# Kernel tuning notes

Hardware: AMD Instinct MI355X
Metric: run time of the kernel (lower is better)

The kernel has to match this reference:

```python
import jax, jax.numpy as jnp
import numpy as np
from jax.scipy.special import logsumexp

N_STATES = 512
N_OBS = 1024
BATCH = 64
T_MAX = 512


def setup_inputs() -> dict:
    key = jax.random.key(0)
    k1, k2, k3, k4, k5 = jax.random.split(key, 5)
    pi = jnp.zeros((N_STATES,), dtype=jnp.float32)
    A = jax.random.normal(k1, (N_STATES, N_STATES), dtype=jnp.float32)  # unnormalized transition
    E = jax.random.normal(k2, (N_STATES, N_OBS), dtype=jnp.float32)     # unnormalized emission
    x = jax.random.randint(k3, (BATCH, T_MAX), 0, N_OBS)
    T = jax.random.randint(k4, (BATCH,), 1, T_MAX + 1)
    return {"pi": pi, "A": A, "E": E, "x": x, "T": T}


def reference(pi, A, E, x, T):
    # log p(x) via forward algorithm in log domain.
    log_pi = jax.nn.log_softmax(pi)                # (N,)
    log_A = jax.nn.log_softmax(A, axis=0)          # (N,N), matches torch dim=0
    log_E = jax.nn.log_softmax(E, axis=1)          # (N,M)

    # emission log-probs per timestep: (B, T_max, N)
    log_em = jnp.moveaxis(log_E[:, x], 0, -1)

    alpha0 = log_em[:, 0, :] + log_pi              # (B,N)

    def step(carry, em_t):
        # carry: (B,N) over k; log_A: (N_i, N_k)
        # next[b,i] = em_t[b,i] + logsumexp_k(log_A[i,k] + carry[b,k])
        nxt = em_t + logsumexp(log_A[None, :, :] + carry[:, None, :], axis=2)
        return nxt, nxt

    em_rest = jnp.swapaxes(log_em[:, 1:, :], 0, 1)  # (T_max-1, B, N)
    _, alphas = jax.lax.scan(step, alpha0, em_rest)
    log_alpha = jnp.concatenate([alpha0[:, None, :], jnp.swapaxes(alphas, 0, 1)], axis=1)  # (B,T_max,N)

    log_sums = logsumexp(log_alpha, axis=2)         # (B, T_max)
    log_probs = jnp.take_along_axis(log_sums, (T - 1)[:, None], axis=1)  # (B,1)
    return log_probs
```

## Files before the change

kernel.cpp:

```cpp
#include <hip/hip_runtime.h>
#include <math.h>

#define NS   512
#define NO   1024
#define NB   64
#define TMAX 512

#define QREG 45
#define QLDS 19

typedef _Float16 h2v __attribute__((ext_vector_type(2)));

__device__ inline float wave_red_sum(float x) {
#pragma unroll
  for (int o = 32; o; o >>= 1) x += __shfl_xor(x, o, 64);
  return x;
}
__device__ inline float wave_red_max(float x) {
#pragma unroll
  for (int o = 32; o; o >>= 1) x = fmaxf(x, __shfl_xor(x, o, 64));
  return x;
}

__device__ inline float dot2u(unsigned int a, unsigned int b, float c) {
#if __has_builtin(__builtin_amdgcn_fdot2)
  return __builtin_amdgcn_fdot2(__builtin_bit_cast(h2v, a),
                                __builtin_bit_cast(h2v, b), c, false);
#else
  h2v av = __builtin_bit_cast(h2v, a), bv = __builtin_bit_cast(h2v, b);
  return c + (float)av.x * (float)bv.x + (float)av.y * (float)bv.y;
#endif
}

__global__ void k_pi(const float* __restrict__ pi, float* __restrict__ pi_sm) {
  __shared__ float red[8];
  int tid = threadIdx.x;
  float v = pi[tid];
  float m = wave_red_max(v);
  if ((tid & 63) == 0) red[tid >> 6] = m;
  __syncthreads();
  m = fmaxf(fmaxf(fmaxf(red[0], red[1]), fmaxf(red[2], red[3])),
            fmaxf(fmaxf(red[4], red[5]), fmaxf(red[6], red[7])));
  float e = __expf(v - m);
  float s = wave_red_sum(e);
  __syncthreads();
  if ((tid & 63) == 0) red[tid >> 6] = s;
  __syncthreads();
  s = red[0] + red[1] + red[2] + red[3] + red[4] + red[5] + red[6] + red[7];
  pi_sm[tid] = e / s;
}

__global__ void k_colLse(const float* __restrict__ A, float* __restrict__ lseA) {
  __shared__ float redm[4];
  __shared__ float reds[4];
  int k = blockIdx.x, tid = threadIdx.x;
  float a0 = A[tid * NS + k], a1 = A[(tid + 256) * NS + k];
  float m = wave_red_max(fmaxf(a0, a1));
  if ((tid & 63) == 0) redm[tid >> 6] = m;
  __syncthreads();
  m = fmaxf(fmaxf(redm[0], redm[1]), fmaxf(redm[2], redm[3]));
  float s = __expf(a0 - m) + __expf(a1 - m);
  s = wave_red_sum(s);
  if ((tid & 63) == 0) reds[tid >> 6] = s;
  __syncthreads();
  s = reds[0] + reds[1] + reds[2] + reds[3];
  if (tid == 0) lseA[k] = m + __logf(s);
}

__global__ void k_rowLseE(const float* __restrict__ E, float* __restrict__ lseE) {
  __shared__ float red[4];
  int i = blockIdx.x, tid = threadIdx.x;
  const float* row = E + i * NO;
  float a0 = row[tid], a1 = row[tid + 256], a2 = row[tid + 512], a3 = row[tid + 768];
  float m = fmaxf(fmaxf(a0, a1), fmaxf(a2, a3));
  m = wave_red_max(m);
  if ((tid & 63) == 0) red[tid >> 6] = m;
  __syncthreads();
  m = fmaxf(fmaxf(red[0], red[1]), fmaxf(red[2], red[3]));
  float s = __expf(a0 - m) + __expf(a1 - m) + __expf(a2 - m) + __expf(a3 - m);
  s = wave_red_sum(s);
  __syncthreads();
  if ((tid & 63) == 0) red[tid >> 6] = s;
  __syncthreads();
  s = red[0] + red[1] + red[2] + red[3];
  if (tid == 0) lseE[i] = m + __logf(s);
}

__global__ void k_pack(const float* __restrict__ A, const float* __restrict__ lseA,
                       unsigned int* __restrict__ W) {
  int u = blockIdx.x * 512 + threadIdx.x;
  int q = u >> 11;
  int r = u & 2047;
  int i = r >> 2;
  int h = r & 3;
  int k0 = q * 8 + h * 2;
  float e0 = __expf(A[i * NS + k0]     - lseA[k0]);
  float e1 = __expf(A[i * NS + k0 + 1] - lseA[k0 + 1]);
  h2v p;
  p.x = (_Float16)e0;
  p.y = (_Float16)e1;
  W[u] = __builtin_bit_cast(unsigned int, p);
}

__global__ __launch_bounds__(512, 1) void k_fwd(
    const float* __restrict__ E, const int* __restrict__ x,
    const int* __restrict__ Tlen, const float* __restrict__ pi_sm,
    const float* __restrict__ lseE, const uint4* __restrict__ Aall,
    float* __restrict__ out) {
  __shared__ uint4 Alds[QLDS * 512];
  __shared__ uint4 vbuf[2][NS / 8];
  __shared__ int xrow[TMAX];
  __shared__ float red[8];
  int b = blockIdx.x, tid = threadIdx.x;

  uint4 areg[QREG];
#pragma unroll
  for (int q = 0; q < QREG; q++) areg[q] = Aall[q * 512 + tid];
#pragma unroll
  for (int q = 0; q < QLDS; q++) Alds[q * 512 + tid] = Aall[(QREG + q) * 512 + tid];

  for (int t = tid; t < TMAX; t += 512) xrow[t] = x[b * TMAX + t];

  float pi_i  = pi_sm[tid];
  float lse_i = lseE[tid];
  const float* Erow = E + tid * NO;
  int Tb = Tlen[b];
  float c = 0.f;
  int cur = 0;
  __syncthreads();

  for (int t = 0; t < Tb; t++) {
    float epre = Erow[xrow[t]];
    float acc;
    if (t == 0) {
      acc = pi_i;
    } else {
      acc = 0.f;
      const uint4* vp = vbuf[cur];
#pragma unroll
      for (int q = 0; q < QREG; q++) {
        uint4 vv = vp[q];
        acc = dot2u(areg[q].x, vv.x, acc);
        acc = dot2u(areg[q].y, vv.y, acc);
        acc = dot2u(areg[q].z, vv.z, acc);
        acc = dot2u(areg[q].w, vv.w, acc);
      }
#pragma unroll
      for (int q = 0; q < QLDS; q++) {
        uint4 av = Alds[q * 512 + tid];
        uint4 vv = vp[QREG + q];
        acc = dot2u(av.x, vv.x, acc);
        acc = dot2u(av.y, vv.y, acc);
        acc = dot2u(av.z, vv.z, acc);
        acc = dot2u(av.w, vv.w, acc);
      }
    }
    float em = __expf(epre - lse_i);
    float nv = acc * em;
    float s = wave_red_sum(nv);
    if ((tid & 63) == 0) red[tid >> 6] = s;
    __syncthreads();
    s = red[0] + red[1] + red[2] + red[3] + red[4] + red[5] + red[6] + red[7];
    c += __logf(s);
    float rs = __builtin_amdgcn_rcpf(s);
    int nxt = cur ^ 1;
    ((_Float16*)vbuf[nxt])[tid] = (_Float16)(nv * rs);
    __syncthreads();
    cur = nxt;
  }
  if (tid == 0) out[b] = c;
}

extern "C" void kernel_launch(void* const* d_in, const int* in_sizes, int n_in,
                              void* d_out, int out_size, void* d_ws, size_t ws_size,
                              hipStream_t stream) {
  const float* pi = (const float*)d_in[0];
  const float* A  = (const float*)d_in[1];
  const float* E  = (const float*)d_in[2];
  const int*   x  = (const int*)d_in[3];
  const int*   T  = (const int*)d_in[4];
  float* out = (float*)d_out;

  char* ws = (char*)d_ws;
  float*        pi_sm = (float*)(ws + 0);
  float*        lseA  = (float*)(ws + 2048);
  float*        lseE  = (float*)(ws + 4096);
  unsigned int* Apk   = (unsigned int*)(ws + 6144);

  hipLaunchKernelGGL(k_pi,      dim3(1),   dim3(512), 0, stream, pi, pi_sm);
  hipLaunchKernelGGL(k_colLse,  dim3(512), dim3(256), 0, stream, A, lseA);
  hipLaunchKernelGGL(k_rowLseE, dim3(512), dim3(256), 0, stream, E, lseE);
  hipLaunchKernelGGL(k_pack,    dim3(256), dim3(512), 0, stream, A, lseA, Apk);
  hipLaunchKernelGGL(k_fwd,     dim3(64),  dim3(512), 0, stream,
                     E, x, T, pi_sm, lseE, (const uint4*)Apk, out);
}
```

Before: 1.018 ms.

## Remove second barrier per step via lagged power-of-two rescaling

Each forward step now writes the unnormalized alpha, scaled by a power of two derived from the previous step's sum, straight into the next fp16 vector. This removes the second __syncthreads per timestep. The normalizer sum is double-buffered and read one step later, and the log-likelihood is accumulated in log2 with a lagged correction. The dot product is split into four independent accumulators to shorten the FMA dependency chain, and the launch bounds and waves_per_eu attributes are adjusted. Exponent-only scaling lets fp16 values range more widely than exact normalization, which risks precision loss.

Result: slower. 1.507 ms (+48.0%).

```diff
diff --git a/kernel.cpp b/kernel.cpp
--- a/kernel.cpp
+++ b/kernel.cpp
@@ -102,7 +102,9 @@
   W[u] = __builtin_bit_cast(unsigned int, p);
 }
 
-__global__ __launch_bounds__(512, 1) void k_fwd(
+__global__ __launch_bounds__(512)
+__attribute__((amdgpu_waves_per_eu(2, 2)))
+void k_fwd(
     const float* __restrict__ E, const int* __restrict__ x,
     const int* __restrict__ Tlen, const float* __restrict__ pi_sm,
     const float* __restrict__ lseE, const uint4* __restrict__ Aall,
@@ -110,12 +112,17 @@
   __shared__ uint4 Alds[QLDS * 512];
   __shared__ uint4 vbuf[2][NS / 8];
   __shared__ int xrow[TMAX];
-  __shared__ float red[8];
+  __shared__ __align__(16) float red[2][8];
   int b = blockIdx.x, tid = threadIdx.x;
 
   uint4 areg[QREG];
 #pragma unroll
   for (int q = 0; q < QREG; q++) areg[q] = Aall[q * 512 + tid];
+#pragma unroll
+  for (int q = 0; q < QREG; q++) {
+    asm volatile("" : "+v"(areg[q].x), "+v"(areg[q].y),
+                      "+v"(areg[q].z), "+v"(areg[q].w));
+  }
 #pragma unroll
   for (int q = 0; q < QLDS; q++) Alds[q * 512 + tid] = Aall[(QREG + q) * 512 + tid];
 
@@ -126,49 +133,68 @@
   const float* Erow = E + tid * NO;
   int Tb = Tlen[b];
   float c = 0.f;
+  float Dlog = 0.f;
+  int gexp_prev = 19;
   int cur = 0;
   __syncthreads();
 
   for (int t = 0; t < Tb; t++) {
+    int nxt = cur ^ 1;
     float epre = Erow[xrow[t]];
+    int gexpw;
+    if (t == 0) {
+      gexpw = 19;
+    } else {
+      const float4* rp = (const float4*)red[cur];
+      float4 ra = rp[0], rb = rp[1];
+      float sp = ((ra.x + ra.y) + (ra.z + ra.w)) + ((rb.x + rb.y) + (rb.z + rb.w));
+      float ls = __log2f(sp);
+      int e = ((__builtin_bit_cast(int, sp) >> 23) & 0xff) - 126;
+      c += ls - Dlog;
+      Dlog = (float)gexp_prev + ls;
+      gexpw = 19 - gexp_prev - e;
+    }
     float acc;
     if (t == 0) {
       acc = pi_i;
     } else {
-      acc = 0.f;
+      float a0 = 0.f, a1 = 0.f, a2 = 0.f, a3 = 0.f;
       const uint4* vp = vbuf[cur];
 #pragma unroll
       for (int q = 0; q < QREG; q++) {
         uint4 vv = vp[q];
-        acc = dot2u(areg[q].x, vv.x, acc);
-        acc = dot2u(areg[q].y, vv.y, acc);
-        acc = dot2u(areg[q].z, vv.z, acc);
-        acc = dot2u(areg[q].w, vv.w, acc);
+        a0 = dot2u(areg[q].x, vv.x, a0);
+        a1 = dot2u(areg[q].y, vv.y, a1);
+        a2 = dot2u(areg[q].z, vv.z, a2);
+        a3 = dot2u(areg[q].w, vv.w, a3);
       }
 #pragma unroll
       for (int q = 0; q < QLDS; q++) {
         uint4 av = Alds[q * 512 + tid];
         uint4 vv = vp[QREG + q];
-        acc = dot2u(av.x, vv.x, acc);
-        acc = dot2u(av.y, vv.y, acc);
-        acc = dot2u(av.z, vv.z, acc);
-        acc = dot2u(av.w, vv.w, acc);
+        a0 = dot2u(av.x, vv.x, a0);
+        a1 = dot2u(av.y, vv.y, a1);
+        a2 = dot2u(av.z, vv.z, a2);
+        a3 = dot2u(av.w, vv.w, a3);
       }
+      acc = (a0 + a1) + (a2 + a3);
     }
     float em = __expf(epre - lse_i);
-    float nv = acc * em;
-    float s = wave_red_sum(nv);
-    if ((tid & 63) == 0) red[tid >> 6] = s;
+    float raw = acc * em;
+    ((_Float16*)vbuf[nxt])[tid] = (_Float16)ldexpf(raw, gexpw);
+    float s = wave_red_sum(raw);
+    if ((tid & 63) == 0) red[nxt][tid >> 6] = s;
+    gexp_prev = gexpw;
+    cur = nxt;
     __syncthreads();
-    s = red[0] + red[1] + red[2] + red[3] + red[4] + red[5] + red[6] + red[7];
-    c += __logf(s);
-    float rs = __builtin_amdgcn_rcpf(s);
-    int nxt = cur ^ 1;
-    ((_Float16*)vbuf[nxt])[tid] = (_Float16)(nv * rs);
-    __syncthreads();
-    cur = nxt;
   }
-  if (tid == 0) out[b] = c;
+  {
+    const float4* rp = (const float4*)red[cur];
+    float4 ra = rp[0], rb = rp[1];
+    float sp = ((ra.x + ra.y) + (ra.z + ra.w)) + ((rb.x + rb.y) + (rb.z + rb.w));
+    c += __log2f(sp) - Dlog;
+  }
+  if (tid == 0) out[b] = c * 0.69314718055994530942f;
 }
 
 extern "C" void kernel_launch(void* const* d_in, const int* in_sizes, int n_in,
```
